# Kernel tuning notes

Measured on AMD Instinct MI355X. Metric: run time of the kernel, lower is better.

The kernel has to match this reference:

```python
import jax, jax.numpy as jnp
import numpy as np

H, DH = 8, 64
DIM = 512
INNER = H * DH
GAMMA = 0.01
LAMBDA_REG = 0.001


def _ln(x, g, b, eps=1e-5):
    mu = x.mean(-1, keepdims=True)
    var = x.var(-1, keepdims=True)  # ddof=0, matches torch LayerNorm
    return (x - mu) / jnp.sqrt(var + eps) * g + b


def _proj(x, ln_g, ln_b, W):
    # LayerNorm -> Linear(no bias) -> split heads: [Q,N,DIM] -> [H,Q,N,DH]
    Q, N, _ = x.shape
    y = _ln(x, ln_g, ln_b) @ W
    return jnp.transpose(y.reshape(Q, N, H, DH), (2, 0, 1, 3))


def setup_inputs() -> dict:
    key = jax.random.key(0)
    ks = jax.random.split(key, 10)
    s = 0.02
    return {
        "q": jax.random.normal(ks[0], (16, 512, DIM), jnp.float32),
        "k": jax.random.normal(ks[1], (16, 512, DIM), jnp.float32),
        "v": jax.random.normal(ks[2], (16, 512, DIM), jnp.float32),
        "ln_g": jnp.ones((DIM,), jnp.float32),
        "ln_b": jnp.zeros((DIM,), jnp.float32),
        "W_in": jax.random.normal(ks[3], (DIM, INNER), jnp.float32) * s,
        "wp1_w": jax.random.normal(ks[4], (2 * DH, DH), jnp.float32) * s,
        "wp1_b": jnp.zeros((DH,), jnp.float32),
        "wpln_g": jnp.ones((DH,), jnp.float32),
        "wpln_b": jnp.zeros((DH,), jnp.float32),
        "wp2_w": jax.random.normal(ks[5], (DH, DH // 2), jnp.float32) * s,
        "wp2_b": jnp.zeros((DH // 2,), jnp.float32),
        "wp3_w": jax.random.normal(ks[6], (DH // 2, 3), jnp.float32) * s,
        "wp3_b": jnp.zeros((3,), jnp.float32),
        "temp": jnp.ones((1,), jnp.float32) * 5.0,
        "W_out": jax.random.normal(ks[7], (INNER, DIM), jnp.float32) * s,
        "b_out": jnp.zeros((DIM,), jnp.float32),
    }


def reference(q, k, v, ln_g, ln_b, W_in, wp1_w, wp1_b, wpln_g, wpln_b,
              wp2_w, wp2_b, wp3_w, wp3_b, temp, W_out, b_out):
    sg = jax.lax.stop_gradient
    std1 = lambda x: jnp.std(x, ddof=1)  # torch.std is unbiased

    f_q = _proj(q, ln_g, ln_b, W_in)  # [H,Q,N,DH]
    f_k = _proj(k, ln_g, ln_b, W_in)  # [H,Q,M,DH]
    f_v = _proj(v, ln_g, ln_b, W_in)
    m = f_k.shape[2]

    # --- cosine similarity component (cosine_distance + extra clamp) ---
    dots_raw = jnp.einsum('hqnd,hqmd->hqnm', f_q, f_k)
    n1 = jnp.linalg.norm(f_q, axis=-1, keepdims=True) + 1e-8          # [H,Q,N,1]
    n2 = jnp.linalg.norm(f_k, axis=-1, keepdims=True) + 1e-8          # [H,Q,M,1]
    cosine_sim = jnp.clip(dots_raw / (n1 * jnp.swapaxes(n2, -1, -2)), -0.99, 0.99)

    # --- regularized covariance component ---
    f_kc = f_k - f_k.mean(axis=2, keepdims=True)
    f_qc = f_q - f_q.mean(axis=-1, keepdims=True)
    cov = jnp.einsum('hqnd,hqmd->hqnm', f_qc, f_kc) / (DH ** 0.5 + 1e-8)
    cov = jnp.clip((LAMBDA_REG / max(m, 1)) * cov, -10.0, 10.0)

    # --- margin-based variance component (eval mode: adaptive_gamma == GAMMA) ---
    fqn = f_q / jnp.maximum(jnp.linalg.norm(f_q, axis=-1, keepdims=True), 1e-8)
    fkn = f_k / jnp.maximum(jnp.linalg.norm(f_k, axis=-1, keepdims=True), 1e-8)
    cs = jnp.clip(jnp.einsum('hqnd,hqmd->hqnm', fqn, fkn), -0.99, 0.99)
    margin = jnp.clip(GAMMA - cs, 0.0, 2.0)
    var_comp = jnp.broadcast_to(margin.mean(-1, keepdims=True), cs.shape)

    # --- dynamic weight predictor (dropouts identity in eval) ---
    qg = f_q.mean(axis=(1, 2))                 # [H,DH]
    kg = f_k.mean(axis=(1, 2))
    feats = jnp.concatenate([qg, kg], axis=-1)  # [H,2*DH]
    h1 = jax.nn.relu(_ln(feats @ wp1_w + wp1_b, wpln_g, wpln_b))
    h2 = jax.nn.relu(h1 @ wp2_w + wp2_b)
    logits = jax.nn.softmax(h2 @ wp3_w + wp3_b, axis=-1)  # softmax inside Sequential
    weights = jax.nn.softmax(logits / jnp.clip(temp, 0.1, 20.0), axis=-1)  # [H,3]
    cos_w = weights[:, 0].reshape(H, 1, 1, 1)
    cov_w = weights[:, 1].reshape(H, 1, 1, 1)
    var_w = weights[:, 2].reshape(H, 1, 1, 1)

    # --- global-std rescale + mix + adaptive temperature ---
    cos_s = cosine_sim / (sg(std1(cosine_sim)) + 1e-8)
    cov_s = cov / (sg(std1(cov)) + 1e-8) * 0.1
    var_s = var_comp / (sg(std1(var_comp)) + 1e-8) * 0.1
    dots = cos_w * cos_s + cov_w * cov_s + var_w * var_s
    attn_t = 1.0 + 0.5 * sg(std1(dots))
    dots = dots / jnp.clip(attn_t, 0.5, 5.0)

    out = jnp.einsum('hqnm,hqmd->hqnd', jax.nn.softmax(dots, axis=-1), f_v)
    out = jnp.transpose(out, (1, 2, 0, 3)).reshape(q.shape[0], q.shape[1], INNER)
    return out @ W_out + b_out
```

## Files before the change

kernel.cpp:

```cpp
#include <hip/hip_runtime.h>
#include <math.h>

#define NH 8
#define DHD 64
#define DMODEL 512
#define QB 16
#define SEQ 512
#define NROWS (QB*SEQ)
#define NHQ (NH*QB)
#define KCOV ((float)((0.001/512.0)/(8.0+1e-8)))

typedef __attribute__((ext_vector_type(8))) short short8;
typedef __attribute__((ext_vector_type(8))) unsigned short ushort8v;
typedef __attribute__((ext_vector_type(4))) unsigned short ushort4v;
typedef __attribute__((ext_vector_type(4))) float f32x4;

__device__ __forceinline__ float bf2f(unsigned short u){
  union { unsigned int i; float f; } c; c.i = ((unsigned int)u)<<16; return c.f;
}
__device__ __forceinline__ unsigned short f2bf(float f){
  union { float f; unsigned int i; } c; c.f = f;
  unsigned int u = c.i;
  u += 0x7fffu + ((u>>16)&1u);
  return (unsigned short)(u>>16);
}
__device__ __forceinline__ unsigned cvtpk(float a, float b){
  unsigned r; asm("v_cvt_pk_bf16_f32 %0, %1, %2" : "=v"(r) : "v"(a), "v"(b)); return r;
}
__device__ __forceinline__ float clampf(float x, float lo, float hi){ return fminf(fmaxf(x,lo),hi); }

__device__ __forceinline__ f32x4 MFMA(short8 a, short8 b, f32x4 c){
  return __builtin_amdgcn_mfma_f32_16x16x32_bf16(a, b, c, 0, 0, 0);
}
__device__ __forceinline__ short8 frag_ld(const unsigned short* T, int row, int rowbytes, int kbyte){
  int addr = row*rowbytes + (kbyte ^ ((row&7)<<4));
  return *reinterpret_cast<const short8*>(reinterpret_cast<const char*>(T) + addr);
}
__device__ __forceinline__ void tile_st16(unsigned short* T, int row, int rowbytes, int kbyte, ushort8v v){
  int addr = row*rowbytes + (kbyte ^ ((row&7)<<4));
  *reinterpret_cast<ushort8v*>(reinterpret_cast<char*>(T) + addr) = v;
}

__global__ void __launch_bounds__(256) prep_kernel(
    const float* __restrict__ xq, const float* __restrict__ xk, const float* __restrict__ xv,
    const float* __restrict__ ln_g, const float* __restrict__ ln_b,
    const float* __restrict__ Wi, const float* __restrict__ Wo,
    unsigned short* __restrict__ xln,
    unsigned short* __restrict__ WiT, unsigned short* __restrict__ WoT)
{
  __shared__ float T[64][68];
  int b = blockIdx.x, t = threadIdx.x;
  if (b < 6144){
    int which = b >> 11, rowblk = b & 2047;
    const float* src = which==0 ? xq : (which==1 ? xk : xv);
    int w = t >> 6, lane = t & 63;
    int row = rowblk*4 + w;
    const float* x = src + (size_t)row*DMODEL;
    float4 v1 = *reinterpret_cast<const float4*>(&x[lane*8]);
    float4 v2 = *reinterpret_cast<const float4*>(&x[lane*8+4]);
    float s  = v1.x+v1.y+v1.z+v1.w + v2.x+v2.y+v2.z+v2.w;
    float ss = v1.x*v1.x+v1.y*v1.y+v1.z*v1.z+v1.w*v1.w
             + v2.x*v2.x+v2.y*v2.y+v2.z*v2.z+v2.w*v2.w;
    #pragma unroll
    for (int m=32; m>0; m>>=1){ s += __shfl_xor(s,m,64); ss += __shfl_xor(ss,m,64); }
    float m_ = s*(1.0f/DMODEL);
    float var = ss*(1.0f/DMODEL) - m_*m_;
    float r_ = rsqrtf(var + 1e-5f);
    float4 g1 = *reinterpret_cast<const float4*>(&ln_g[lane*8]);
    float4 g2 = *reinterpret_cast<const float4*>(&ln_g[lane*8+4]);
    float4 b1 = *reinterpret_cast<const float4*>(&ln_b[lane*8]);
    float4 b2 = *reinterpret_cast<const float4*>(&ln_b[lane*8+4]);
    ushort8v o;
    o[0]=f2bf((v1.x-m_)*r_*g1.x + b1.x);
    o[1]=f2bf((v1.y-m_)*r_*g1.y + b1.y);
    o[2]=f2bf((v1.z-m_)*r_*g1.z + b1.z);
    o[3]=f2bf((v1.w-m_)*r_*g1.w + b1.w);
    o[4]=f2bf((v2.x-m_)*r_*g2.x + b2.x);
    o[5]=f2bf((v2.y-m_)*r_*g2.y + b2.y);
    o[6]=f2bf((v2.z-m_)*r_*g2.z + b2.z);
    o[7]=f2bf((v2.w-m_)*r_*g2.w + b2.w);
    *reinterpret_cast<ushort8v*>(&xln[((size_t)which*NROWS + row)*DMODEL + lane*8]) = o;
  } else {
    int wb = b - 6144;
    const float* src = (wb>=64) ? Wo : Wi;
    unsigned short* dst = (wb>=64) ? WoT : WiT;
    int rc = wb & 63;
    int r0 = (rc>>3)*64, c0 = (rc&7)*64;
    for (int it=0; it<4; ++it){
      int idx = it*256+t, row = idx>>4, q = idx&15;
      float4 v = *reinterpret_cast<const float4*>(&src[(size_t)(r0+row)*DMODEL + c0 + q*4]);
      T[row][q*4+0]=v.x; T[row][q*4+1]=v.y; T[row][q*4+2]=v.z; T[row][q*4+3]=v.w;
    }
    __syncthreads();
    for (int it=0; it<4; ++it){
      int idx = it*256+t, oc = idx>>4, q = idx&15;
      ushort4v o;
      o[0]=f2bf(T[q*4+0][oc]); o[1]=f2bf(T[q*4+1][oc]);
      o[2]=f2bf(T[q*4+2][oc]); o[3]=f2bf(T[q*4+3][oc]);
      *reinterpret_cast<ushort4v*>(&dst[(size_t)(c0+oc)*DMODEL + r0 + q*4]) = o;
    }
  }
}

__global__ void __launch_bounds__(256) proj_mfma_kernel(
    const unsigned short* __restrict__ xln,
    const unsigned short* __restrict__ WiT,
    unsigned short* __restrict__ fq, unsigned short* __restrict__ fk, unsigned short* __restrict__ fvT,
    float* __restrict__ aqA, float* __restrict__ i1qA,
    float* __restrict__ rskA, float* __restrict__ i1kA)
{
  int which = blockIdx.z;
  const unsigned short* src = xln + (size_t)which*NROWS*DMODEL;
  int r0 = blockIdx.x*128;
  int c0 = blockIdx.y*128;
  __shared__ unsigned short XT[128*64];
  __shared__ unsigned short WT[128*64];
  int t = threadIdx.x;
  int w=t>>6, lane=t&63, l16=lane&15, lh=lane>>4;
  f32x4 acc[4][4];
  #pragma unroll
  for(int i=0;i<4;i++){ for(int j=0;j<4;j++) acc[i][j]=(f32x4){0.f,0.f,0.f,0.f}; }
  for (int k0=0;k0<DMODEL;k0+=64){
    __syncthreads();
    for (int it=0; it<4; ++it){
      int idx=it*256+t, row=idx>>3, q=idx&7;
      ushort8v v = *reinterpret_cast<const ushort8v*>(&src[(size_t)(r0+row)*DMODEL + k0 + q*8]);
      tile_st16(XT, row, 128, q*16, v);
    }
    for (int it=0; it<4; ++it){
      int idx=it*256+t, row=idx>>3, q=idx&7;
      ushort8v v = *reinterpret_cast<const ushort8v*>(&WiT[(size_t)(c0+row)*DMODEL + k0 + q*8]);
      tile_st16(WT, row, 128, q*16, v);
    }
    __syncthreads();
    if (which<2){
      int dr=(w&1)*64, nc=(w>>1)*64;
      #pragma unroll
      for (int ks=0; ks<2; ++ks){
        int kb = lh*16 + ks*64;
        short8 a[4], b[4];
        #pragma unroll
        for (int i=0;i<4;i++) a[i] = frag_ld(WT, dr+i*16+l16, 128, kb);
        #pragma unroll
        for (int j=0;j<4;j++) b[j] = frag_ld(XT, nc+j*16+l16, 128, kb);
        #pragma unroll
        for (int i=0;i<4;i++){
          #pragma unroll
          for (int j=0;j<4;j++) acc[i][j]=MFMA(a[i],b[j],acc[i][j]);
        }
      }
    } else {
      int nr=(w>>1)*64, dc=(w&1)*64;
      #pragma unroll
      for (int ks=0; ks<2; ++ks){
        int kb = lh*16 + ks*64;
        short8 a[4], b[4];
        #pragma unroll
        for (int i=0;i<4;i++) a[i] = frag_ld(XT, nr+i*16+l16, 128, kb);
        #pragma unroll
        for (int j=0;j<4;j++) b[j] = frag_ld(WT, dc+j*16+l16, 128, kb);
        #pragma unroll
        for (int i=0;i<4;i++){
          #pragma unroll
          for (int j=0;j<4;j++) acc[i][j]=MFMA(a[i],b[j],acc[i][j]);
        }
      }
    }
  }
  if (which<2){
    unsigned short* dst = which ? fk : fq;
    int dr=(w&1)*64, nc=(w>>1)*64;
    #pragma unroll
    for (int i=0;i<4;i++){
      #pragma unroll
      for (int j=0;j<4;j++){
        int cl = c0 + dr + i*16 + lh*4;
        int ng = r0 + nc + j*16 + l16;
        int head = cl>>6, dd = cl&63;
        int hq = head*QB + (ng>>9);
        int n = ng&511;
        ushort4v o;
        o[0]=f2bf(acc[i][j][0]); o[1]=f2bf(acc[i][j][1]);
        o[2]=f2bf(acc[i][j][2]); o[3]=f2bf(acc[i][j][3]);
        *reinterpret_cast<ushort4v*>(&dst[((size_t)hq*SEQ+n)*DHD + dd]) = o;
      }
    }
    int head = (c0>>6) + (w&1);
    #pragma unroll
    for (int j=0;j<4;j++){
      float s=0.f, ss=0.f;
      #pragma unroll
      for (int i=0;i<4;i++){
        #pragma unroll
        for (int r=0;r<4;r++){ float x = acc[i][j][r]; s += x; ss = fmaf(x,x,ss); }
      }
      s += __shfl_xor(s,16,64); ss += __shfl_xor(ss,16,64);
      s += __shfl_xor(s,32,64); ss += __shfl_xor(ss,32,64);
      if (lh==0){
        int ng = r0 + nc + j*16 + l16;
        int hq = head*QB + (ng>>9);
        int n = ng&511;
        float nrm = sqrtf(ss);
        if (which==0){
          aqA[hq*SEQ+n]  = s*(1.0f/64.0f);
          i1qA[hq*SEQ+n] = 1.0f/(nrm+1e-8f);
        } else {
          rskA[hq*SEQ+n] = s;
          i1kA[hq*SEQ+n] = 1.0f/(nrm+1e-8f);
        }
      }
    }
  } else {
    int nr=(w>>1)*64, dc=(w&1)*64;
    #pragma unroll
    for (int i=0;i<4;i++){
      #pragma unroll
      for (int j=0;j<4;j++){
        int ngb = r0 + nr + i*16 + lh*4;
        int dg  = c0 + dc + j*16 + l16;
        int head = dg>>6, dd = dg&63;
        int hq = head*QB + (ngb>>9);
        int n = ngb&511;
        ushort4v o;
        o[0]=f2bf(acc[i][j][0]); o[1]=f2bf(acc[i][j][1]);
        o[2]=f2bf(acc[i][j][2]); o[3]=f2bf(acc[i][j][3]);
        *reinterpret_cast<ushort4v*>(&fvT[((size_t)hq*DHD+dd)*SEQ + n]) = o;
      }
    }
  }
}

__global__ void __launch_bounds__(256) colstat_kernel(
    const unsigned short* __restrict__ fq, const unsigned short* __restrict__ fk,
    float* __restrict__ qgp, float* __restrict__ kgp, float* __restrict__ c2A)
{
  int hq = blockIdx.x, isk = blockIdx.y;
  const unsigned short* F = (isk ? fk : fq) + (size_t)hq*SEQ*DHD;
  int t = threadIdx.x, g = t&15, rg = t>>4;
  float acc0=0.f, acc1=0.f, acc2=0.f, acc3=0.f;
  #pragma unroll 4
  for (int i=0;i<32;i++){
    int r = rg + 16*i;
    ushort4v v = *reinterpret_cast<const ushort4v*>(&F[(size_t)r*DHD + g*4]);
    acc0+=bf2f(v[0]); acc1+=bf2f(v[1]); acc2+=bf2f(v[2]); acc3+=bf2f(v[3]);
  }
  __shared__ float sh[16][68];
  sh[rg][g*4+0]=acc0; sh[rg][g*4+1]=acc1; sh[rg][g*4+2]=acc2; sh[rg][g*4+3]=acc3;
  __syncthreads();
  if (t<64){
    float s=0.f;
    #pragma unroll
    for (int r=0;r<16;r++) s += sh[r][t];
    if (isk){
      kgp[hq*64+t]=s;
      float c = s*(1.0f/512.0f);
      #pragma unroll
      for (int m=32;m>0;m>>=1) c += __shfl_xor(c,m,64);
      if (t==0) c2A[hq]=c;
    } else {
      qgp[hq*64+t]=s;
    }
  }
}

__global__ void __launch_bounds__(256) score_m1_kernel(
    const unsigned short* __restrict__ fq, const unsigned short* __restrict__ fk,
    const float* __restrict__ aqA, const float* __restrict__ i1qA,
    const float* __restrict__ rskA, const float* __restrict__ i1kA,
    const float* __restrict__ c2A, const float* __restrict__ kgp,
    float* __restrict__ c1A, float* __restrict__ rmaxcA, float* __restrict__ rmaxoA,
    float* __restrict__ momf, double* __restrict__ varp)
{
  int strip=blockIdx.x, q_=blockIdx.y, h=blockIdx.z;
  int hq=h*QB+q_, n0=strip*64;
  const unsigned short* Fq=fq+(size_t)hq*SEQ*DHD;
  const unsigned short* Fk=fk+(size_t)hq*SEQ*DHD;
  __shared__ unsigned short KT[128*64];
  __shared__ float rskL[512], i1kL[512];
  __shared__ float red[256];
  __shared__ double dred[256];
  int t=threadIdx.x, w=t>>6, lane=t&63, l16=lane&15, lh=lane>>4;
  int n = n0 + w*16 + l16;
  for (int i=t;i<512;i+=256){ rskL[i]=rskA[hq*SEQ+i]; i1kL[i]=i1kA[hq*SEQ+i]; }
  float c2v = c2A[hq];
  float aqv = aqA[hq*SEQ+n];
  float iq1 = i1qA[hq*SEQ+n];
  short8 qa[2];
  #pragma unroll
  for (int ks=0;ks<2;ks++)
    qa[ks] = *reinterpret_cast<const short8*>(&Fq[(size_t)n*DHD + ks*32 + lh*8]);
  float c1v = 0.f;
  #pragma unroll
  for (int ks=0;ks<2;ks++){
    const float* bkp = &kgp[hq*64 + ks*32 + lh*8];
    float4 b0 = *reinterpret_cast<const float4*>(bkp);
    float4 b1 = *reinterpret_cast<const float4*>(bkp+4);
    float bb[8] = {b0.x,b0.y,b0.z,b0.w,b1.x,b1.y,b1.z,b1.w};
    #pragma unroll
    for (int i=0;i<8;i++) c1v = fmaf(bf2f((unsigned short)qa[ks][i]), bb[i], c1v);
  }
  c1v *= (1.0f/512.0f);
  c1v += __shfl_xor(c1v,16,64);
  c1v += __shfl_xor(c1v,32,64);
  if (lane<16) c1A[hq*SEQ+n] = c1v;
  float c1x = KCOV*(c1v - aqv*c2v);
  float aqx = KCOV*aqv;
  float sc=0.f,sc2=0.f,so=0.f,so2=0.f,sco=0.f;
  float rc=0.f, ro=0.f, rm=0.f, rmc=-1e30f, rmo=-1e30f;
  for (int mc=0;mc<4;mc++){
    int m0=mc*128;
    __syncthreads();
    for (int it=0;it<4;++it){
      int idx=it*256+t, row=idx>>3, qc=idx&7;
      ushort8v vv = *reinterpret_cast<const ushort8v*>(&Fk[(size_t)(m0+row)*DHD + qc*8]);
      tile_st16(KT,row,128,qc*16,vv);
    }
    __syncthreads();
    #pragma unroll
    for (int mh=0;mh<2;mh++){
      int mb = mh*64;
      f32x4 acc[4];
      #pragma unroll
      for (int mf=0;mf<4;mf++) acc[mf]=(f32x4){0.f,0.f,0.f,0.f};
      #pragma unroll
      for (int mf=0;mf<4;mf++){
        #pragma unroll
        for (int ks=0;ks<2;ks++){
          short8 kf = frag_ld(KT, mb+mf*16+l16, 128, lh*16+ks*64);
          acc[mf] = MFMA(kf, qa[ks], acc[mf]);
        }
      }
      #pragma unroll
      for (int mf=0;mf<4;mf++){
        int ml = m0 + mb + mf*16 + lh*4;
        float4 rsk4 = *reinterpret_cast<const float4*>(&rskL[ml]);
        float4 i1k4 = *reinterpret_cast<const float4*>(&i1kL[ml]);
        float rk[4]={rsk4.x,rsk4.y,rsk4.z,rsk4.w};
        float ik[4]={i1k4.x,i1k4.y,i1k4.z,i1k4.w};
        #pragma unroll
        for (int r=0;r<4;r++){
          float S = acc[mf][r];
          float cosv = clampf(S*iq1*ik[r], -0.99f, 0.99f);
          float u = fmaf(KCOV, S, -c1x);
          float covv = fmaf(-aqx, rk[r], u);
          covv = clampf(covv, -10.0f, 10.0f);
          float marg = clampf(0.01f - cosv, 0.0f, 2.0f);
          sc += cosv; sc2 = fmaf(cosv,cosv,sc2);
          so += covv; so2 = fmaf(covv,covv,so2);
          sco = fmaf(cosv,covv,sco);
          rc += cosv; ro += covv; rm += marg;
          rmc = fmaxf(rmc, cosv); rmo = fmaxf(rmo, covv);
        }
      }
    }
  }
  rc += __shfl_xor(rc,16,64); rc += __shfl_xor(rc,32,64);
  ro += __shfl_xor(ro,16,64); ro += __shfl_xor(ro,32,64);
  rm += __shfl_xor(rm,16,64); rm += __shfl_xor(rm,32,64);
  rmc = fmaxf(rmc, __shfl_xor(rmc,16,64)); rmc = fmaxf(rmc, __shfl_xor(rmc,32,64));
  rmo = fmaxf(rmo, __shfl_xor(rmo,16,64)); rmo = fmaxf(rmo, __shfl_xor(rmo,32,64));
  if (lane<16){
    rmaxcA[hq*SEQ+n] = rmc;
    rmaxoA[hq*SEQ+n] = rmo;
  }
  double vm=0.0, vm2=0.0, vmc=0.0, vmo=0.0;
  if (lane<16){
    float mm = rm*(1.0f/512.0f);
    vm  = (double)mm;
    vm2 = (double)mm*(double)mm;
    vmc = (double)mm*(double)rc;
    vmo = (double)mm*(double)ro;
  }
  float fs[5]={sc,sc2,so,so2,sco};
  for (int c=0;c<5;c++){
    __syncthreads();
    red[t]=fs[c]; __syncthreads();
    for (int o=128;o>0;o>>=1){ if (t<o) red[t]+=red[t+o]; __syncthreads(); }
    if (t==0) momf[(size_t)(hq*8+strip)*5 + c] = red[0];
  }
  double ds[4]={vm,vm2,vmc,vmo};
  for (int c=0;c<4;c++){
    __syncthreads();
    dred[t]=ds[c]; __syncthreads();
    for (int o=128;o>0;o>>=1){ if (t<o) dred[t]+=dred[t+o]; __syncthreads(); }
    if (t==0) varp[(size_t)(hq*8+strip)*4 + c] = dred[0];
  }
}

__global__ void __launch_bounds__(256) finalize_kernel(
    const float* __restrict__ qgp, const float* __restrict__ kgp,
    const float* __restrict__ wp1w, const float* __restrict__ wp1b,
    const float* __restrict__ wplg, const float* __restrict__ wplb,
    const float* __restrict__ wp2w, const float* __restrict__ wp2b,
    const float* __restrict__ wp3w, const float* __restrict__ wp3b,
    const float* __restrict__ temp,
    const float* __restrict__ momf, const double* __restrict__ varp,
    float* __restrict__ params)
{
  int t = threadIdx.x;
  __shared__ float feats[8][128];
  __shared__ float h1s[8][64];
  __shared__ float h2s[8][32];
  __shared__ float wts[8][3];
  __shared__ double Sh[8][9];
  for (int idx=t; idx<512; idx+=256){
    int h = idx>>6, d = idx&63;
    float s1=0, s2=0;
    for (int qq=0; qq<QB; qq++){ s1 += qgp[(h*QB+qq)*64+d]; s2 += kgp[(h*QB+qq)*64+d]; }
    feats[h][d]    = s1*(1.0f/8192.0f);
    feats[h][64+d] = s2*(1.0f/8192.0f);
  }
  __syncthreads();
  int w = t>>6, j = t&63;
  for (int pp=0; pp<2; pp++){
    int h = w + pp*4;
    float acc = wp1b[j];
    for (int k=0;k<128;k++) acc += feats[h][k]*wp1w[k*64+j];
    float s=acc, s2=acc*acc;
    #pragma unroll
    for (int m=32;m>0;m>>=1){ s+=__shfl_xor(s,m,64); s2+=__shfl_xor(s2,m,64); }
    float mean = s*(1.0f/64.0f);
    float var  = s2*(1.0f/64.0f) - mean*mean;
    float xh = (acc-mean)*rsqrtf(var+1e-5f)*wplg[j] + wplb[j];
    h1s[h][j] = fmaxf(xh, 0.0f);
  }
  __syncthreads();
  {
    int h = t>>5, j2 = t&31;
    float acc = wp2b[j2];
    for (int k=0;k<64;k++) acc += h1s[h][k]*wp2w[k*32+j2];
    h2s[h][j2] = fmaxf(acc, 0.0f);
  }
  __syncthreads();
  if (t<8){
    int h = t;
    float z[3] = {wp3b[0], wp3b[1], wp3b[2]};
    for (int k=0;k<32;k++){
      float hv = h2s[h][k];
      z[0]+=hv*wp3w[k*3]; z[1]+=hv*wp3w[k*3+1]; z[2]+=hv*wp3w[k*3+2];
    }
    float mx = fmaxf(z[0], fmaxf(z[1], z[2]));
    float e0=expf(z[0]-mx), e1=expf(z[1]-mx), e2=expf(z[2]-mx);
    float inv = 1.0f/(e0+e1+e2);
    float l0=e0*inv, l1=e1*inv, l2=e2*inv;
    float tv = temp[0]; tv = fminf(fmaxf(tv, 0.1f), 20.0f);
    float y0=l0/tv, y1=l1/tv, y2=l2/tv;
    float mx2 = fmaxf(y0, fmaxf(y1, y2));
    float f0=expf(y0-mx2), f1=expf(y1-mx2), f2=expf(y2-mx2);
    float inv2 = 1.0f/(f0+f1+f2);
    wts[h][0]=f0*inv2; wts[h][1]=f1*inv2; wts[h][2]=f2*inv2;
  }
  __syncthreads();
  if (t<40){
    int h = t/5, c = t%5;
    double s = 0;
    for (int e=0; e<128; e++) s += (double)momf[(size_t)(h*128+e)*5 + c];
    Sh[h][c] = s;
  }
  __syncthreads();
  if (t<32){
    int h = t>>2, c = t&3;
    double s = 0;
    for (int e=0; e<128; e++) s += varp[(size_t)(h*128+e)*4 + c];
    Sh[h][5+c] = s;
  }
  __syncthreads();
  if (t==0){
    const double Ntot = 33554432.0;
    double T1c=0,T2c=0,T1o=0,T2o=0,T1v=0,T2v=0;
    for (int h=0;h<8;h++){
      T1c+=Sh[h][0]; T2c+=Sh[h][1]; T1o+=Sh[h][2]; T2o+=Sh[h][3];
      T1v+=512.0*Sh[h][5]; T2v+=512.0*Sh[h][6];
    }
    double stdc = sqrt(fmax((T2c - T1c*T1c/Ntot)/(Ntot-1.0), 0.0));
    double stdo = sqrt(fmax((T2o - T1o*T1o/Ntot)/(Ntot-1.0), 0.0));
    double stdv = sqrt(fmax((T2v - T1v*T1v/Ntot)/(Ntot-1.0), 0.0));
    double ah[8], bh[8];
    double Sd1=0, Sd2=0;
    for (int h=0;h<8;h++){
      double a = (double)wts[h][0]/(stdc+1e-8);
      double b = (double)wts[h][1]*0.1/(stdo+1e-8);
      double c = (double)wts[h][2]*0.1/(stdv+1e-8);
      ah[h]=a; bh[h]=b;
      Sd1 += a*Sh[h][0] + b*Sh[h][2] + c*512.0*Sh[h][5];
      Sd2 += a*a*Sh[h][1] + b*b*Sh[h][3] + c*c*512.0*Sh[h][6]
           + 2.0*a*b*Sh[h][4] + 2.0*a*c*Sh[h][7] + 2.0*b*c*Sh[h][8];
    }
    double stdd = sqrt(fmax((Sd2 - Sd1*Sd1/Ntot)/(Ntot-1.0), 0.0));
    double att = 1.0 + 0.5*stdd;
    att = fmin(fmax(att, 0.5), 5.0);
    double scale = 1.0/att;
    for (int h=0;h<8;h++){
      params[h*2+0] = (float)(scale*ah[h]);
      params[h*2+1] = (float)(scale*bh[h]);
    }
  }
}

__global__ void __launch_bounds__(256) attn_m2_kernel(
    const unsigned short* __restrict__ fq, const unsigned short* __restrict__ fk,
    const unsigned short* __restrict__ fvT,
    const float* __restrict__ aqA, const float* __restrict__ c1A, const float* __restrict__ i1qA,
    const float* __restrict__ rskA, const float* __restrict__ i1kA,
    const float* __restrict__ c2A, const float* __restrict__ params,
    const float* __restrict__ rmaxcA, const float* __restrict__ rmaxoA,
    unsigned short* __restrict__ attn_bf)
{
  int strip=blockIdx.x, q_=blockIdx.y, h=blockIdx.z;
  int hq=h*QB+q_, n0=strip*64;
  const unsigned short* Fq=fq+(size_t)hq*SEQ*DHD;
  const unsigned short* Fk=fk+(size_t)hq*SEQ*DHD;
  const unsigned short* FvT=fvT+(size_t)hq*DHD*SEQ;
  __shared__ unsigned short KT[128*64];
  __shared__ unsigned short VT[64*128];
  __shared__ unsigned short P[64*64];
  __shared__ float rskL[512], i1kL[512];
  int t=threadIdx.x, w=t>>6, lane=t&63, l16=lane&15, lh=lane>>4;
  int n = n0 + w*16 + l16;
  for (int i=t;i<512;i+=256){ rskL[i]=rskA[hq*SEQ+i]; i1kL[i]=i1kA[hq*SEQ+i]; }
  float c2v=c2A[hq];
  float pa=params[h*2], pb=params[h*2+1];
  float aqv = aqA[hq*SEQ+n];
  float c1v = c1A[hq*SEQ+n];
  float iq1 = i1qA[hq*SEQ+n];
  float rmc = rmaxcA[hq*SEQ+n];
  float rmo = rmaxoA[hq*SEQ+n];
  float pbk = pb*KCOV;
  float ra  = pa*iq1;
  float bndc = 0.99f*pa;
  float rowc = -pbk*(c1v - aqv*c2v);
  float r3   = pbk*aqv;
  float Mrow = fmaf(pa, rmc, pb*rmo);
  short8 qa[2];
  #pragma unroll
  for (int ks=0;ks<2;ks++)
    qa[ks] = *reinterpret_cast<const short8*>(&Fq[(size_t)n*DHD + ks*32 + lh*8]);
  short8 ones;
  #pragma unroll
  for (int i=0;i<8;i++) ones[i] = (short)0x3F80;
  f32x4 accO[4];
  #pragma unroll
  for (int j=0;j<4;j++) accO[j]=(f32x4){0.f,0.f,0.f,0.f};
  f32x4 den = (f32x4){0.f,0.f,0.f,0.f};
  for (int mc=0;mc<4;mc++){
    int m0=mc*128;
    __syncthreads();
    for (int it=0;it<4;++it){
      int idx=it*256+t, row=idx>>3, qc=idx&7;
      ushort8v vv = *reinterpret_cast<const ushort8v*>(&Fk[(size_t)(m0+row)*DHD + qc*8]);
      tile_st16(KT,row,128,qc*16,vv);
    }
    for (int it=0;it<4;++it){
      int idx=it*256+t, dd=idx>>4, c=idx&15;
      ushort8v vv=*reinterpret_cast<const ushort8v*>(&FvT[(size_t)dd*SEQ + m0 + c*8]);
      tile_st16(VT, dd, 256, c*16, vv);
    }
    __syncthreads();
    #pragma unroll
    for (int mh=0;mh<2;mh++){
      int mb = mh*64;
      f32x4 acc[4];
      #pragma unroll
      for (int mf=0;mf<4;mf++) acc[mf]=(f32x4){0.f,0.f,0.f,0.f};
      #pragma unroll
      for (int mf=0;mf<4;mf++){
        #pragma unroll
        for (int ks=0;ks<2;ks++){
          short8 kf = frag_ld(KT, mb+mf*16+l16, 128, lh*16+ks*64);
          acc[mf] = MFMA(kf, qa[ks], acc[mf]);
        }
      }
      int prow = w*16 + l16;
      #pragma unroll
      for (int mf=0;mf<4;mf++){
        int ml = m0 + mb + mf*16 + lh*4;
        float4 rsk4 = *reinterpret_cast<const float4*>(&rskL[ml]);
        float4 i1k4 = *reinterpret_cast<const float4*>(&i1kL[ml]);
        float rk[4]={rsk4.x,rsk4.y,rsk4.z,rsk4.w};
        float ik[4]={i1k4.x,i1k4.y,i1k4.z,i1k4.w};
        #pragma unroll
        for (int r=0;r<4;r++){
          float S = acc[mf][r];
          float tt = S*ra; tt *= ik[r];
          float cc = clampf(tt, -bndc, bndc);
          float u = fmaf(pbk, S, rowc);
          float lin = fmaf(-r3, rk[r], u);
          acc[mf][r] = __expf(cc + lin - Mrow);
        }
        unsigned lo = cvtpk(acc[mf][0], acc[mf][1]);
        unsigned hi = cvtpk(acc[mf][2], acc[mf][3]);
        int pbyte = (mf*32 + lh*8) ^ ((prow&7)<<4);
        *reinterpret_cast<uint2*>(reinterpret_cast<char*>(P) + prow*128 + pbyte)
          = make_uint2(lo, hi);
      }
      #pragma unroll
      for (int ks=0;ks<2;ks++){
        short8 pfrag = frag_ld(P, prow, 128, lh*16 + ks*64);
        #pragma unroll
        for (int dcf=0;dcf<4;dcf++){
          short8 vb = frag_ld(VT, dcf*16+l16, 256, mb*2 + ks*64 + lh*16);
          accO[dcf] = MFMA(pfrag, vb, accO[dcf]);
        }
        den = MFMA(pfrag, ones, den);
      }
    }
  }
  f32x4 invD;
  #pragma unroll
  for (int r=0;r<4;r++) invD[r] = 1.0f/den[r];
  #pragma unroll
  for (int dcf=0;dcf<4;dcf++){
    #pragma unroll
    for (int r=0;r<4;r++){
      int row = w*16 + lh*4 + r;
      int col = dcf*16 + l16;
      int addr = row*128 + ((col*2) ^ ((row&7)<<4));
      *reinterpret_cast<unsigned short*>(reinterpret_cast<char*>(P) + addr)
        = f2bf(accO[dcf][r]*invD[r]);
    }
  }
  __syncthreads();
  for (int it=0; it<2; ++it){
    int idx = it*256 + t;
    int row = idx>>3, c = idx&7;
    int addr = row*128 + ((c*16) ^ ((row&7)<<4));
    ushort8v vv = *reinterpret_cast<ushort8v*>(reinterpret_cast<char*>(P) + addr);
    *reinterpret_cast<ushort8v*>(
      &attn_bf[(size_t)(q_*SEQ + n0 + row)*DMODEL + h*DHD + c*8]) = vv;
  }
}

__global__ void __launch_bounds__(256) out_mfma_kernel(
    const unsigned short* __restrict__ attn_bf, const unsigned short* __restrict__ WoT,
    const float* __restrict__ bias, float* __restrict__ out)
{
  int r0=blockIdx.x*128;
  int c0=blockIdx.y*128;
  __shared__ unsigned short AT[128*64];
  __shared__ unsigned short WT[128*64];
  int t=threadIdx.x, w=t>>6, lane=t&63, l16=lane&15, lh=lane>>4;
  f32x4 acc[4][4];
  #pragma unroll
  for(int i=0;i<4;i++){ for(int j=0;j<4;j++) acc[i][j]=(f32x4){0.f,0.f,0.f,0.f}; }
  for (int k0=0;k0<DMODEL;k0+=64){
    __syncthreads();
    for (int it=0; it<4; ++it){
      int idx=it*256+t, row=idx>>3, q=idx&7;
      ushort8v v = *reinterpret_cast<const ushort8v*>(&attn_bf[(size_t)(r0+row)*DMODEL + k0 + q*8]);
      tile_st16(AT, row, 128, q*16, v);
    }
    for (int it=0; it<4; ++it){
      int idx=it*256+t, row=idx>>3, q=idx&7;
      ushort8v v = *reinterpret_cast<const ushort8v*>(&WoT[(size_t)(c0+row)*DMODEL + k0 + q*8]);
      tile_st16(WT, row, 128, q*16, v);
    }
    __syncthreads();
    int nr=(w&1)*64, mr=(w>>1)*64;
    #pragma unroll
    for (int ks=0; ks<2; ++ks){
      int kb = lh*16 + ks*64;
      short8 a[4], b[4];
      #pragma unroll
      for (int i=0;i<4;i++) a[i] = frag_ld(WT, nr+i*16+l16, 128, kb);
      #pragma unroll
      for (int j=0;j<4;j++) b[j] = frag_ld(AT, mr+j*16+l16, 128, kb);
      #pragma unroll
      for (int i=0;i<4;i++){
        #pragma unroll
        for (int j=0;j<4;j++) acc[i][j]=MFMA(a[i],b[j],acc[i][j]);
      }
    }
  }
  #pragma unroll
  for (int i=0;i<4;i++){
    int nb = c0+(w&1)*64+i*16+lh*4;
    float4 b4 = *reinterpret_cast<const float4*>(&bias[nb]);
    #pragma unroll
    for (int j=0;j<4;j++){
      int mg = r0+(w>>1)*64+j*16+l16;
      f32x4 o = acc[i][j];
      o[0]+=b4.x; o[1]+=b4.y; o[2]+=b4.z; o[3]+=b4.w;
      *reinterpret_cast<f32x4*>(&out[(size_t)mg*DMODEL + nb]) = o;
    }
  }
}

extern "C" void kernel_launch(void* const* d_in, const int* in_sizes, int n_in,
                              void* d_out, int out_size, void* d_ws, size_t ws_size,
                              hipStream_t stream)
{
  (void)in_sizes; (void)n_in; (void)out_size; (void)ws_size;
  const float* q     = (const float*)d_in[0];
  const float* k     = (const float*)d_in[1];
  const float* v     = (const float*)d_in[2];
  const float* ln_g  = (const float*)d_in[3];
  const float* ln_b  = (const float*)d_in[4];
  const float* W_in  = (const float*)d_in[5];
  const float* wp1w  = (const float*)d_in[6];
  const float* wp1b  = (const float*)d_in[7];
  const float* wplg  = (const float*)d_in[8];
  const float* wplb  = (const float*)d_in[9];
  const float* wp2w  = (const float*)d_in[10];
  const float* wp2b  = (const float*)d_in[11];
  const float* wp3w  = (const float*)d_in[12];
  const float* wp3b  = (const float*)d_in[13];
  const float* temp  = (const float*)d_in[14];
  const float* W_out = (const float*)d_in[15];
  const float* b_out = (const float*)d_in[16];
  float* out = (float*)d_out;

  char* wsb = (char*)d_ws;
  size_t off = 0;
  auto alloc = [&](size_t bytes)->char*{
    char* p = wsb + off; off += (bytes + 255) & ~(size_t)255; return p;
  };
  unsigned short* xln    = (unsigned short*)alloc((size_t)3*NROWS*DMODEL*2);
  unsigned short* fq_b   = (unsigned short*)alloc((size_t)NHQ*SEQ*DHD*2);
  unsigned short* fk_b   = (unsigned short*)alloc((size_t)NHQ*SEQ*DHD*2);
  unsigned short* fvT_b  = (unsigned short*)alloc((size_t)NHQ*SEQ*DHD*2);
  unsigned short* attn_b = (unsigned short*)alloc((size_t)NROWS*DMODEL*2);
  unsigned short* WiT    = (unsigned short*)alloc((size_t)DMODEL*DMODEL*2);
  unsigned short* WoT    = (unsigned short*)alloc((size_t)DMODEL*DMODEL*2);
  float* aqA    = (float*)alloc(NHQ*SEQ*4);
  float* c1A    = (float*)alloc(NHQ*SEQ*4);
  float* i1qA   = (float*)alloc(NHQ*SEQ*4);
  float* rskA   = (float*)alloc(NHQ*SEQ*4);
  float* i1kA   = (float*)alloc(NHQ*SEQ*4);
  float* rmaxcA = (float*)alloc(NHQ*SEQ*4);
  float* rmaxoA = (float*)alloc(NHQ*SEQ*4);
  float* c2A    = (float*)alloc(NHQ*4);
  float* qgp    = (float*)alloc(NHQ*64*4);
  float* kgp    = (float*)alloc(NHQ*64*4);
  float* momf   = (float*)alloc((size_t)NHQ*8*5*4);
  double* varp  = (double*)alloc((size_t)NHQ*8*4*8);
  float* params = (float*)alloc(64);

  prep_kernel<<<6272, 256, 0, stream>>>(q, k, v, ln_g, ln_b, W_in, W_out, xln, WiT, WoT);
  proj_mfma_kernel<<<dim3(64,4,3), 256, 0, stream>>>(xln, WiT, fq_b, fk_b, fvT_b,
                                                     aqA, i1qA, rskA, i1kA);
  colstat_kernel<<<dim3(NHQ, 2), 256, 0, stream>>>(fq_b, fk_b, qgp, kgp, c2A);
  score_m1_kernel<<<dim3(8, QB, NH), 256, 0, stream>>>(fq_b, fk_b, aqA, i1qA, rskA, i1kA,
                                                       c2A, kgp, c1A, rmaxcA, rmaxoA, momf, varp);
  finalize_kernel<<<1, 256, 0, stream>>>(qgp, kgp, wp1w, wp1b, wplg, wplb, wp2w, wp2b,
                                         wp3w, wp3b, temp, momf, varp, params);
  attn_m2_kernel<<<dim3(8, QB, NH), 256, 0, stream>>>(fq_b, fk_b, fvT_b, aqA, c1A, i1qA,
                                                      rskA, i1kA, c2A, params, rmaxcA, rmaxoA, attn_b);
  out_mfma_kernel<<<dim3(64,4), 256, 0, stream>>>(attn_b, WoT, b_out, out);
}
```

Before: 169.6 us.

## Load K and V MFMA fragments directly from global memory instead of LDS tiles

Both the score and attention kernels stop staging K and V tiles in shared memory and read MFMA fragments straight from global (L2/L1-cached) memory. The 128-row chunk loop with its barriers is flattened into an 8-step loop over 64-row chunks. Occupancy hints of 6 blocks per CU are added to both kernels. This removes the LDS staging traffic and barriers and lowers LDS use so more blocks fit, at the cost of more scattered, less coalesced global loads that each wave issues redundantly. The P buffer in the attention kernel is still written and read within each iteration with no barrier between chunks, which may be a race.

```diff
diff --git a/kernel.cpp b/kernel.cpp
--- a/kernel.cpp
+++ b/kernel.cpp
@@ -263,7 +263,7 @@
   }
 }
 
-__global__ void __launch_bounds__(256) score_m1_kernel(
+__global__ void __launch_bounds__(256,6) score_m1_kernel(
     const unsigned short* __restrict__ fq, const unsigned short* __restrict__ fk,
     const float* __restrict__ aqA, const float* __restrict__ i1qA,
     const float* __restrict__ rskA, const float* __restrict__ i1kA,
@@ -275,7 +275,6 @@
   int hq=h*QB+q_, n0=strip*64;
   const unsigned short* Fq=fq+(size_t)hq*SEQ*DHD;
   const unsigned short* Fk=fk+(size_t)hq*SEQ*DHD;
-  __shared__ unsigned short KT[128*64];
   __shared__ float rskL[512], i1kL[512];
   __shared__ float red[256];
   __shared__ double dred[256];
@@ -305,52 +304,43 @@
   if (lane<16) c1A[hq*SEQ+n] = c1v;
   float c1x = KCOV*(c1v - aqv*c2v);
   float aqx = KCOV*aqv;
+  __syncthreads();
   float sc=0.f,sc2=0.f,so=0.f,so2=0.f,sco=0.f;
   float rc=0.f, ro=0.f, rm=0.f, rmc=-1e30f, rmo=-1e30f;
-  for (int mc=0;mc<4;mc++){
-    int m0=mc*128;
-    __syncthreads();
-    for (int it=0;it<4;++it){
-      int idx=it*256+t, row=idx>>3, qc=idx&7;
-      ushort8v vv = *reinterpret_cast<const ushort8v*>(&Fk[(size_t)(m0+row)*DHD + qc*8]);
-      tile_st16(KT,row,128,qc*16,vv);
-    }
-    __syncthreads();
-    #pragma unroll
-    for (int mh=0;mh<2;mh++){
-      int mb = mh*64;
-      f32x4 acc[4];
-      #pragma unroll
-      for (int mf=0;mf<4;mf++) acc[mf]=(f32x4){0.f,0.f,0.f,0.f};
-      #pragma unroll
-      for (int mf=0;mf<4;mf++){
-        #pragma unroll
-        for (int ks=0;ks<2;ks++){
-          short8 kf = frag_ld(KT, mb+mf*16+l16, 128, lh*16+ks*64);
-          acc[mf] = MFMA(kf, qa[ks], acc[mf]);
-        }
-      }
-      #pragma unroll
-      for (int mf=0;mf<4;mf++){
-        int ml = m0 + mb + mf*16 + lh*4;
-        float4 rsk4 = *reinterpret_cast<const float4*>(&rskL[ml]);
-        float4 i1k4 = *reinterpret_cast<const float4*>(&i1kL[ml]);
-        float rk[4]={rsk4.x,rsk4.y,rsk4.z,rsk4.w};
-        float ik[4]={i1k4.x,i1k4.y,i1k4.z,i1k4.w};
-        #pragma unroll
-        for (int r=0;r<4;r++){
-          float S = acc[mf][r];
-          float cosv = clampf(S*iq1*ik[r], -0.99f, 0.99f);
-          float u = fmaf(KCOV, S, -c1x);
-          float covv = fmaf(-aqx, rk[r], u);
-          covv = clampf(covv, -10.0f, 10.0f);
-          float marg = clampf(0.01f - cosv, 0.0f, 2.0f);
-          sc += cosv; sc2 = fmaf(cosv,cosv,sc2);
-          so += covv; so2 = fmaf(covv,covv,so2);
-          sco = fmaf(cosv,covv,sco);
-          rc += cosv; ro += covv; rm += marg;
-          rmc = fmaxf(rmc, cosv); rmo = fmaxf(rmo, covv);
-        }
+  for (int mc=0;mc<8;mc++){
+    int mb = mc*64;
+    f32x4 acc[4];
+    #pragma unroll
+    for (int mf=0;mf<4;mf++) acc[mf]=(f32x4){0.f,0.f,0.f,0.f};
+    #pragma unroll
+    for (int mf=0;mf<4;mf++){
+      #pragma unroll
+      for (int ks=0;ks<2;ks++){
+        short8 kf = *reinterpret_cast<const short8*>(
+            &Fk[(size_t)(mb+mf*16+l16)*DHD + ks*32 + lh*8]);
+        acc[mf] = MFMA(kf, qa[ks], acc[mf]);
+      }
+    }
+    #pragma unroll
+    for (int mf=0;mf<4;mf++){
+      int ml = mb + mf*16 + lh*4;
+      float4 rsk4 = *reinterpret_cast<const float4*>(&rskL[ml]);
+      float4 i1k4 = *reinterpret_cast<const float4*>(&i1kL[ml]);
+      float rk[4]={rsk4.x,rsk4.y,rsk4.z,rsk4.w};
+      float ik[4]={i1k4.x,i1k4.y,i1k4.z,i1k4.w};
+      #pragma unroll
+      for (int r=0;r<4;r++){
+        float S = acc[mf][r];
+        float cosv = clampf(S*iq1*ik[r], -0.99f, 0.99f);
+        float u = fmaf(KCOV, S, -c1x);
+        float covv = fmaf(-aqx, rk[r], u);
+        covv = clampf(covv, -10.0f, 10.0f);
+        float marg = clampf(0.01f - cosv, 0.0f, 2.0f);
+        sc += cosv; sc2 = fmaf(cosv,cosv,sc2);
+        so += covv; so2 = fmaf(covv,covv,so2);
+        sco = fmaf(cosv,covv,sco);
+        rc += cosv; ro += covv; rm += marg;
+        rmc = fmaxf(rmc, cosv); rmo = fmaxf(rmo, covv);
       }
     }
   }
@@ -497,7 +487,7 @@
   }
 }
 
-__global__ void __launch_bounds__(256) attn_m2_kernel(
+__global__ void __launch_bounds__(256,6) attn_m2_kernel(
     const unsigned short* __restrict__ fq, const unsigned short* __restrict__ fk,
     const unsigned short* __restrict__ fvT,
     const float* __restrict__ aqA, const float* __restrict__ c1A, const float* __restrict__ i1qA,
@@ -511,8 +501,6 @@
   const unsigned short* Fq=fq+(size_t)hq*SEQ*DHD;
   const unsigned short* Fk=fk+(size_t)hq*SEQ*DHD;
   const unsigned short* FvT=fvT+(size_t)hq*DHD*SEQ;
-  __shared__ unsigned short KT[128*64];
-  __shared__ unsigned short VT[64*128];
   __shared__ unsigned short P[64*64];
   __shared__ float rskL[512], i1kL[512];
   int t=threadIdx.x, w=t>>6, lane=t&63, l16=lane&15, lh=lane>>4;
@@ -542,67 +530,54 @@
   #pragma unroll
   for (int j=0;j<4;j++) accO[j]=(f32x4){0.f,0.f,0.f,0.f};
   f32x4 den = (f32x4){0.f,0.f,0.f,0.f};
-  for (int mc=0;mc<4;mc++){
-    int m0=mc*128;
-    __syncthreads();
-    for (int it=0;it<4;++it){
-      int idx=it*256+t, row=idx>>3, qc=idx&7;
-      ushort8v vv = *reinterpret_cast<const ushort8v*>(&Fk[(size_t)(m0+row)*DHD + qc*8]);
-      tile_st16(KT,row,128,qc*16,vv);
-    }
-    for (int it=0;it<4;++it){
-      int idx=it*256+t, dd=idx>>4, c=idx&15;
-      ushort8v vv=*reinterpret_cast<const ushort8v*>(&FvT[(size_t)dd*SEQ + m0 + c*8]);
-      tile_st16(VT, dd, 256, c*16, vv);
-    }
-    __syncthreads();
-    #pragma unroll
-    for (int mh=0;mh<2;mh++){
-      int mb = mh*64;
-      f32x4 acc[4];
-      #pragma unroll
-      for (int mf=0;mf<4;mf++) acc[mf]=(f32x4){0.f,0.f,0.f,0.f};
-      #pragma unroll
-      for (int mf=0;mf<4;mf++){
-        #pragma unroll
-        for (int ks=0;ks<2;ks++){
-          short8 kf = frag_ld(KT, mb+mf*16+l16, 128, lh*16+ks*64);
-          acc[mf] = MFMA(kf, qa[ks], acc[mf]);
-        }
-      }
-      int prow = w*16 + l16;
-      #pragma unroll
-      for (int mf=0;mf<4;mf++){
-        int ml = m0 + mb + mf*16 + lh*4;
-        float4 rsk4 = *reinterpret_cast<const float4*>(&rskL[ml]);
-        float4 i1k4 = *reinterpret_cast<const float4*>(&i1kL[ml]);
-        float rk[4]={rsk4.x,rsk4.y,rsk4.z,rsk4.w};
-        float ik[4]={i1k4.x,i1k4.y,i1k4.z,i1k4.w};
-        #pragma unroll
-        for (int r=0;r<4;r++){
-          float S = acc[mf][r];
-          float tt = S*ra; tt *= ik[r];
-          float cc = clampf(tt, -bndc, bndc);
-          float u = fmaf(pbk, S, rowc);
-          float lin = fmaf(-r3, rk[r], u);
-          acc[mf][r] = __expf(cc + lin - Mrow);
-        }
-        unsigned lo = cvtpk(acc[mf][0], acc[mf][1]);
-        unsigned hi = cvtpk(acc[mf][2], acc[mf][3]);
-        int pbyte = (mf*32 + lh*8) ^ ((prow&7)<<4);
-        *reinterpret_cast<uint2*>(reinterpret_cast<char*>(P) + prow*128 + pbyte)
-          = make_uint2(lo, hi);
-      }
+  __syncthreads();
+  int prow = w*16 + l16;
+  for (int mc=0;mc<8;mc++){
+    int mb = mc*64;
+    f32x4 acc[4];
+    #pragma unroll
+    for (int mf=0;mf<4;mf++) acc[mf]=(f32x4){0.f,0.f,0.f,0.f};
+    #pragma unroll
+    for (int mf=0;mf<4;mf++){
       #pragma unroll
       for (int ks=0;ks<2;ks++){
-        short8 pfrag = frag_ld(P, prow, 128, lh*16 + ks*64);
-        #pragma unroll
-        for (int dcf=0;dcf<4;dcf++){
-          short8 vb = frag_ld(VT, dcf*16+l16, 256, mb*2 + ks*64 + lh*16);
-          accO[dcf] = MFMA(pfrag, vb, accO[dcf]);
-        }
-        den = MFMA(pfrag, ones, den);
-      }
+        short8 kf = *reinterpret_cast<const short8*>(
+            &Fk[(size_t)(mb+mf*16+l16)*DHD + ks*32 + lh*8]);
+        acc[mf] = MFMA(kf, qa[ks], acc[mf]);
+      }
+    }
+    #pragma unroll
+    for (int mf=0;mf<4;mf++){
+      int ml = mb + mf*16 + lh*4;
+      float4 rsk4 = *reinterpret_cast<const float4*>(&rskL[ml]);
+      float4 i1k4 = *reinterpret_cast<const float4*>(&i1kL[ml]);
+      float rk[4]={rsk4.x,rsk4.y,rsk4.z,rsk4.w};
+      float ik[4]={i1k4.x,i1k4.y,i1k4.z,i1k4.w};
+      #pragma unroll
+      for (int r=0;r<4;r++){
+        float S = acc[mf][r];
+        float tt = S*ra; tt *= ik[r];
+        float cc = clampf(tt, -bndc, bndc);
+        float u = fmaf(pbk, S, rowc);
+        float lin = fmaf(-r3, rk[r], u);
+        acc[mf][r] = __expf(cc + lin - Mrow);
+      }
+      unsigned lo = cvtpk(acc[mf][0], acc[mf][1]);
+      unsigned hi = cvtpk(acc[mf][2], acc[mf][3]);
+      int pbyte = (mf*32 + lh*8) ^ ((prow&7)<<4);
+      *reinterpret_cast<uint2*>(reinterpret_cast<char*>(P) + prow*128 + pbyte)
+        = make_uint2(lo, hi);
+    }
+    #pragma unroll
+    for (int ks=0;ks<2;ks++){
+      short8 pfrag = frag_ld(P, prow, 128, lh*16 + ks*64);
+      #pragma unroll
+      for (int dcf=0;dcf<4;dcf++){
+        short8 vb = *reinterpret_cast<const short8*>(
+            &FvT[(size_t)(dcf*16+l16)*SEQ + mb + ks*32 + lh*8]);
+        accO[dcf] = MFMA(pfrag, vb, accO[dcf]);
+      }
+      den = MFMA(pfrag, ones, den);
     }
   }
   f32x4 invD;
```

Measured after the change: 193.9 us. 1.14x slower.
